# Optimization experiments

Hardware: AMD Instinct MI355X
Metric: run time of the kernel (lower is better)

## Reference

```python
import jax, jax.numpy as jnp
import numpy as np

B, S, D = 4, 1024, 1024
H = 16           # heads
HD = D // H      # head dim
E = 8            # experts
TOPK = 2
F = 4 * D        # expert ffn hidden


def setup_inputs() -> dict:
    key = jax.random.key(0)
    ks = jax.random.split(key, 8)
    w = lambda k, shp: jax.random.normal(k, shp, dtype=jnp.float32) * 0.02
    return {
        "x": jax.random.normal(ks[0], (B, S, D), dtype=jnp.float32),
        "ln1_g": jnp.ones((D,), jnp.float32), "ln1_b": jnp.zeros((D,), jnp.float32),
        "Wqkv": w(ks[1], (D, 3 * D)),
        "Wo": w(ks[2], (D, D)),
        "ln2_g": jnp.ones((D,), jnp.float32), "ln2_b": jnp.zeros((D,), jnp.float32),
        "Wg": w(ks[3], (D, E)),
        "W1": w(ks[4], (E, D, F)),
        "W2": w(ks[5], (E, F, D)),
    }


def _layernorm(x, g, b, eps=1e-5):
    mu = jnp.mean(x, axis=-1, keepdims=True)
    var = jnp.var(x, axis=-1, keepdims=True)
    return (x - mu) * jax.lax.rsqrt(var + eps) * g + b


def _attn(h, Wqkv, Wo):
    qkv = h @ Wqkv                                   # [B,S,3D]
    q, k, v = jnp.split(qkv, 3, axis=-1)
    q = q.reshape(B, S, H, HD)
    k = k.reshape(B, S, H, HD)
    v = v.reshape(B, S, H, HD)
    scores = jnp.einsum("bqhd,bkhd->bhqk", q, k) / np.sqrt(HD)
    causal = jnp.tril(jnp.ones((S, S), bool))
    scores = jnp.where(causal, scores, jnp.finfo(scores.dtype).min)
    p = jax.nn.softmax(scores, axis=-1)
    o = jnp.einsum("bhqk,bkhd->bqhd", p, v).reshape(B, S, D)
    return o @ Wo


def _moe(h, Wg, W1, W2):
    # h: [N, D] tokens; top-k softmax gating, dense all-expert reference
    logits = h @ Wg                                   # [N, E]
    top_vals, top_idx = jax.lax.top_k(logits, TOPK)   # [N, k]
    wts = jax.nn.softmax(top_vals, axis=-1)           # gate weights over top-k
    gates = jnp.sum(jax.nn.one_hot(top_idx, E) * wts[..., None], axis=1)  # [N, E]
    act = jax.nn.gelu(jnp.einsum("nd,edf->enf", h, W1))  # [E, N, F]
    eo = jnp.einsum("enf,efd->end", act, W2)             # [E, N, D]
    return jnp.einsum("ne,end->nd", gates, eo)           # combine


def reference(x, ln1_g, ln1_b, Wqkv, Wo, ln2_g, ln2_b, Wg, W1, W2):
    h = _layernorm(x, ln1_g, ln1_b)
    x_resid = x + _attn(h, Wqkv, Wo)
    moe_in = _layernorm(x_resid, ln2_g, ln2_b).reshape(B * S, D)
    y = _moe(moe_in, Wg, W1, W2).reshape(B, S, D)
    return x_resid + y
```

## Files before the change

kernel.cpp:

```cpp
#include <hip/hip_runtime.h>

typedef unsigned short u16;
typedef _Float16 f16x8 __attribute__((ext_vector_type(8)));
typedef __bf16   bf16x8 __attribute__((ext_vector_type(8)));
typedef float    f32x4 __attribute__((ext_vector_type(4)));

struct __align__(8) U16x4 { u16 v[4]; };

#define MAXT 72

__device__ __forceinline__ u16 f2b(float f) {
  unsigned u = __builtin_bit_cast(unsigned, f);
  return (u16)((u + 0x7FFFu + ((u >> 16) & 1u)) >> 16);
}
__device__ __forceinline__ u16 f2h(float f) { return __builtin_bit_cast(u16, (_Float16)f); }
__device__ __forceinline__ u16 f2h_lo(float f) {
  _Float16 h = (_Float16)f;
  return __builtin_bit_cast(u16, (_Float16)(f - (float)h));
}
__device__ __forceinline__ void llds16(const void* g, void* l) {
  __builtin_amdgcn_global_load_lds((const __attribute__((address_space(1))) unsigned int*)g,
                                   (__attribute__((address_space(3))) unsigned int*)l, 16, 0, 0);
}
__device__ __forceinline__ f32x4 mmf(f16x8 a, f16x8 b, f32x4 c) {
  return __builtin_amdgcn_mfma_f32_16x16x32_f16(a, b, c, 0, 0, 0);
}
__device__ __forceinline__ f32x4 mmb(bf16x8 a, bf16x8 b, f32x4 c) {
  return __builtin_amdgcn_mfma_f32_16x16x32_bf16(a, b, c, 0, 0, 0);
}

template<int OUT>
__global__ __launch_bounds__(256) void transpose_kernel(const float* __restrict__ src,
                                                        u16* __restrict__ d0, u16* __restrict__ d1,
                                                        int R, int C) {
  __shared__ float t[32][33];
  long zo = (long)blockIdx.z * R * C;
  int r0 = blockIdx.y << 5, c0 = blockIdx.x << 5;
  int tid = threadIdx.x;
  {
    int r = tid >> 3, c = (tid & 7) << 2;
    float4 v = *(const float4*)(src + zo + (long)(r0 + r) * C + c0 + c);
    t[r][c] = v.x; t[r][c + 1] = v.y; t[r][c + 2] = v.z; t[r][c + 3] = v.w;
  }
  __syncthreads();
  int c = tid >> 3, rg = (tid & 7) << 2;
  long o = zo + (long)(c0 + c) * R + r0 + rg;
  U16x4 a, b2;
#pragma unroll
  for (int i = 0; i < 4; i++) {
    float f = t[rg + i][c];
    if (OUT == 0) { a.v[i] = f2h(f); b2.v[i] = f2h_lo(f); }
    else a.v[i] = f2b(f);
  }
  *(U16x4*)(d0 + o) = a;
  if (OUT == 0) *(U16x4*)(d1 + o) = b2;
}

__global__ __launch_bounds__(256) void wg_transpose(const float* __restrict__ Wg,
                                                    float* __restrict__ WgT) {
  int idx = blockIdx.x * 256 + threadIdx.x;
  int d = idx >> 3, e = idx & 7;
  WgT[e * 1024 + d] = Wg[idx];
}

__global__ __launch_bounds__(256) void ln_kernel(const float* __restrict__ x, const float* __restrict__ g,
                                                 const float* __restrict__ bt,
                                                 u16* __restrict__ d0, u16* __restrict__ d1) {
  long row = blockIdx.x;
  int tid = threadIdx.x;
  const float4 v = *(const float4*)(x + (row << 10) + (tid << 2));
  float s = v.x + v.y + v.z + v.w;
  float q = v.x * v.x + v.y * v.y + v.z * v.z + v.w * v.w;
#pragma unroll
  for (int m = 1; m < 64; m <<= 1) { s += __shfl_xor(s, m); q += __shfl_xor(q, m); }
  __shared__ float rs[4], rq[4];
  if ((tid & 63) == 0) { rs[tid >> 6] = s; rq[tid >> 6] = q; }
  __syncthreads();
  s = rs[0] + rs[1] + rs[2] + rs[3];
  q = rq[0] + rq[1] + rq[2] + rq[3];
  float mu = s * (1.f / 1024.f);
  float inv = 1.f / sqrtf(q * (1.f / 1024.f) - mu * mu + 1e-5f);
  float4 gg = *(const float4*)(g + (tid << 2));
  float4 bb = *(const float4*)(bt + (tid << 2));
  float o0 = (v.x - mu) * inv * gg.x + bb.x;
  float o1 = (v.y - mu) * inv * gg.y + bb.y;
  float o2 = (v.z - mu) * inv * gg.z + bb.z;
  float o3 = (v.w - mu) * inv * gg.w + bb.w;
  long o = (row << 10) + (tid << 2);
  U16x4 a, b2;
  a.v[0] = f2h(o0); a.v[1] = f2h(o1); a.v[2] = f2h(o2); a.v[3] = f2h(o3);
  b2.v[0] = f2h_lo(o0); b2.v[1] = f2h_lo(o1); b2.v[2] = f2h_lo(o2); b2.v[3] = f2h_lo(o3);
  *(U16x4*)(d0 + o) = a; *(U16x4*)(d1 + o) = b2;
}

template<int MODE>
__global__ __launch_bounds__(512, 1) void gemm_kernel(
    const u16* __restrict__ Ah, const u16* __restrict__ Al,
    const u16* __restrict__ Bh, const u16* __restrict__ Bl,
    int K, int ldc, int Nexp,
    const int* __restrict__ lists, const int* __restrict__ tile_e,
    const int* __restrict__ tile_b, const int* __restrict__ tile_c,
    float* __restrict__ outf, u16* __restrict__ outb,
    const float* __restrict__ resid, const float* __restrict__ slotw) {
  constexpr bool SPLIT = (MODE < 2);
  constexpr int TN = (MODE == 1) ? 64 : 128;
  constexpr int NF = TN >> 6;
  constexpr int NB = TN >> 6;
  __shared__ u16 lds[4][8192];
  const int tid = threadIdx.x, w = tid >> 6, l = tid & 63;
  int n0;
  int grbase = 0, rowsv = 128;
  long m0 = 0;
  if (MODE >= 2) {
    int lin = blockIdx.x;
    int c = lin & 7, k = lin >> 3;
    int ty = c * 9 + (k % 9);
    int tx = k / 9;
    n0 = tx * TN;
    int e = tile_e[ty];
    if (e < 0) return;
    grbase = tile_b[ty];
    rowsv = tile_c[ty];
    Bh += (long)e * Nexp * K;
  } else {
    n0 = blockIdx.x * TN;
    m0 = (long)blockIdx.y << 7;
  }

  const u16 *as0[2], *as1[2], *bs0[2], *bs1[2];
  int dstA[2], dstB[2];
#pragma unroll
  for (int i = 0; i < 2; i++) {
    int chunk = i * 512 + tid;
    int row = chunk >> 3, c16 = chunk & 7;
    int scol = (c16 << 4) ^ ((row & 7) << 4);
    dstA[i] = chunk << 4;
    long ar;
    if (MODE == 2) {
      int vlu = lists[(row < rowsv) ? (grbase + row) : grbase];
      ar = (long)(vlu >> 1);
    } else if (MODE == 3) {
      ar = grbase + ((row < rowsv) ? row : 0);
    } else {
      ar = m0 + row;
    }
    long ao = ar * (long)K + (scol >> 1);
    as0[i] = Ah + ao;
    if (SPLIT) as1[i] = Al + ao;
  }
#pragma unroll
  for (int i = 0; i < NB; i++) {
    int chunk = i * 512 + tid;
    int row = chunk >> 3, c16 = chunk & 7;
    int scol = (c16 << 4) ^ ((row & 7) << 4);
    dstB[i] = chunk << 4;
    long bo = (long)(n0 + row) * K + (scol >> 1);
    bs0[i] = Bh + bo;
    if (SPLIT) bs1[i] = Bl + bo;
  }

  f32x4 acc[4][NF];
#pragma unroll
  for (int i = 0; i < 4; i++)
#pragma unroll
    for (int j = 0; j < NF; j++) acc[i][j] = (f32x4){0.f, 0.f, 0.f, 0.f};

  const int wr = (w >> 2) << 6;
  const int wc = (w & 3) * (TN / 4);
  const int nkt = K >> 6;

  if constexpr (SPLIT) {
    for (int kt = 0; kt < nkt; ++kt) {
      if (kt) __syncthreads();
#pragma unroll
      for (int i = 0; i < 2; i++) {
        llds16(as0[i] + (kt << 6), (char*)(&lds[0][0]) + dstA[i]);
        llds16(as1[i] + (kt << 6), (char*)(&lds[2][0]) + dstA[i]);
      }
#pragma unroll
      for (int i = 0; i < NB; i++) {
        llds16(bs0[i] + (kt << 6), (char*)(&lds[1][0]) + dstB[i]);
        llds16(bs1[i] + (kt << 6), (char*)(&lds[3][0]) + dstB[i]);
      }
      __syncthreads();
#pragma unroll
      for (int kc = 0; kc < 2; kc++) {
        const int kby = (kc << 6) + ((l >> 4) << 4);
        int aoff[4], boff[NF];
#pragma unroll
        for (int mf = 0; mf < 4; mf++) { int row = wr + (mf << 4) + (l & 15); aoff[mf] = (row << 7) + (kby ^ ((row & 7) << 4)); }
#pragma unroll
        for (int nf = 0; nf < NF; nf++) { int row = wc + (nf << 4) + (l & 15); boff[nf] = (row << 7) + (kby ^ ((row & 7) << 4)); }
        f16x8 a0[4], a1[4], b0[NF], b1[NF];
#pragma unroll
        for (int mf = 0; mf < 4; mf++) {
          a0[mf] = *(const f16x8*)((const char*)(&lds[0][0]) + aoff[mf]);
          a1[mf] = *(const f16x8*)((const char*)(&lds[2][0]) + aoff[mf]);
        }
#pragma unroll
        for (int nf = 0; nf < NF; nf++) {
          b0[nf] = *(const f16x8*)((const char*)(&lds[1][0]) + boff[nf]);
          b1[nf] = *(const f16x8*)((const char*)(&lds[3][0]) + boff[nf]);
        }
#pragma unroll
        for (int mf = 0; mf < 4; mf++)
#pragma unroll
          for (int nf = 0; nf < NF; nf++) {
            acc[mf][nf] = mmf(a0[mf], b0[nf], acc[mf][nf]);
            acc[mf][nf] = mmf(a0[mf], b1[nf], acc[mf][nf]);
            acc[mf][nf] = mmf(a1[mf], b0[nf], acc[mf][nf]);
          }
      }
    }
  } else {
#pragma unroll
    for (int i = 0; i < 2; i++) llds16(as0[i], (char*)(&lds[0][0]) + dstA[i]);
#pragma unroll
    for (int i = 0; i < NB; i++) llds16(bs0[i], (char*)(&lds[1][0]) + dstB[i]);
    __syncthreads();
    int cur = 0;
    for (int kt = 0; kt < nkt; ++kt) {
      if (kt + 1 < nkt) {
        const int nb = (cur ^ 1) << 1;
#pragma unroll
        for (int i = 0; i < 2; i++) llds16(as0[i] + ((kt + 1) << 6), (char*)(&lds[nb][0]) + dstA[i]);
#pragma unroll
        for (int i = 0; i < NB; i++) llds16(bs0[i] + ((kt + 1) << 6), (char*)(&lds[nb + 1][0]) + dstB[i]);
      }
      const char* pA = (const char*)(&lds[cur << 1][0]);
      const char* pB = (const char*)(&lds[(cur << 1) + 1][0]);
#pragma unroll
      for (int kc = 0; kc < 2; kc++) {
        const int kby = (kc << 6) + ((l >> 4) << 4);
        bf16x8 a0[4], b0[NF];
#pragma unroll
        for (int mf = 0; mf < 4; mf++) {
          int row = wr + (mf << 4) + (l & 15);
          a0[mf] = *(const bf16x8*)(pA + (row << 7) + (kby ^ ((row & 7) << 4)));
        }
#pragma unroll
        for (int nf = 0; nf < NF; nf++) {
          int row = wc + (nf << 4) + (l & 15);
          b0[nf] = *(const bf16x8*)(pB + (row << 7) + (kby ^ ((row & 7) << 4)));
        }
#pragma unroll
        for (int mf = 0; mf < 4; mf++)
#pragma unroll
          for (int nf = 0; nf < NF; nf++) acc[mf][nf] = mmb(a0[mf], b0[nf], acc[mf][nf]);
      }
      __syncthreads();
      cur ^= 1;
    }
  }

#pragma unroll
  for (int mf = 0; mf < 4; mf++) {
#pragma unroll
    for (int r = 0; r < 4; r++) {
      const int lrow = wr + (mf << 4) + ((l >> 4) << 2) + r;
      if (MODE >= 2 && lrow >= rowsv) continue;
      float gw = 0.f; long orow = 0;
      if (MODE == 3) { int gr = grbase + lrow; orow = (long)lists[gr] * ldc; gw = slotw[gr]; }
#pragma unroll
      for (int nf = 0; nf < NF; nf++) {
        const int col = n0 + wc + (nf << 4) + (l & 15);
        float v = acc[mf][nf][r];
        if (MODE == 0) {
          outf[(m0 + lrow) * (long)ldc + col] = v;
        } else if (MODE == 1) {
          long ix = (m0 + lrow) * (long)ldc + col;
          outf[ix] = v + resid[ix];
        } else if (MODE == 2) {
          float t = v * (1.59576912f + 0.07135539f * v * v);
          float u = v * __builtin_amdgcn_rcpf(1.f + __expf(-t));
          outb[(long)(grbase + lrow) * ldc + col] = f2b(u);
        } else {
          outf[orow + col] = v * gw;
        }
      }
    }
  }
}

__global__ __launch_bounds__(256) void kv_prep(const float* __restrict__ qkv,
                                               u16* __restrict__ Kh, u16* __restrict__ Kl,
                                               u16* __restrict__ Vth, u16* __restrict__ Vtl) {
  __shared__ float t[64][65];
  const int tid = threadIdx.x;
  const int kb = blockIdx.x, h = blockIdx.y, b = blockIdx.z;
  const long bb = ((long)b) << 10;
  const int hoff = h << 6;
  const long head = ((long)(b * 16 + h)) << 16;
  {
    int rr = tid >> 4, c = (tid & 15) << 2;
#pragma unroll
    for (int p = 0; p < 4; p++) {
      int r = rr + p * 16;
      const float* base = qkv + (bb + kb * 64 + r) * 3072 + hoff + c;
      float4 u = *(const float4*)(base + 1024);
      U16x4 a, lo;
      a.v[0] = f2h(u.x); a.v[1] = f2h(u.y); a.v[2] = f2h(u.z); a.v[3] = f2h(u.w);
      lo.v[0] = f2h_lo(u.x); lo.v[1] = f2h_lo(u.y); lo.v[2] = f2h_lo(u.z); lo.v[3] = f2h_lo(u.w);
      long o = head + (long)(kb * 64 + r) * 64 + c;
      *(U16x4*)(Kh + o) = a; *(U16x4*)(Kl + o) = lo;
      float4 v = *(const float4*)(base + 2048);
      t[r][c] = v.x; t[r][c + 1] = v.y; t[r][c + 2] = v.z; t[r][c + 3] = v.w;
    }
  }
  __syncthreads();
  {
    int hd = tid >> 2, k4 = (tid & 3) << 4;
#pragma unroll
    for (int q = 0; q < 4; q++) {
      U16x4 a, lo;
#pragma unroll
      for (int j = 0; j < 4; j++) {
        float f = t[k4 + q * 4 + j][hd];
        a.v[j] = f2h(f); lo.v[j] = f2h_lo(f);
      }
      long o = head + (long)hd * 1024 + kb * 64 + k4 + q * 4;
      *(U16x4*)(Vth + o) = a; *(U16x4*)(Vtl + o) = lo;
    }
  }
}

__global__ __launch_bounds__(256, 1) void attn_kernel(const float* __restrict__ qkv,
                                                      const u16* __restrict__ Kh, const u16* __restrict__ Kl,
                                                      const u16* __restrict__ Vth, const u16* __restrict__ Vtl,
                                                      u16* __restrict__ oh, u16* __restrict__ ol) {
  __shared__ u16 kh[4096], kl[4096];
  __shared__ u16 vh[4096], vl[4096];
  __shared__ u16 ph[4][1024], pl[4][1024];
  const int tid = threadIdx.x, w = tid >> 6, l = tid & 63;
  const int qbi = blockIdx.x, hh_ = blockIdx.y, b = blockIdx.z;
  const long bb = ((long)b) << 10;
  const int hoff = hh_ << 6;
  const long head = ((long)(b * 16 + hh_)) << 16;

  const u16 *ks0[2], *ks1[2], *vs0[2], *vs1[2];
  int db[2];
#pragma unroll
  for (int i = 0; i < 2; i++) {
    int chunk = i * 256 + tid;
    int row = chunk >> 3, c16 = chunk & 7;
    int sc = ((c16 << 4) ^ ((row & 7) << 4)) >> 1;
    db[i] = chunk << 4;
    ks0[i] = Kh + head + row * 64 + sc;
    ks1[i] = Kl + head + row * 64 + sc;
    vs0[i] = Vth + head + (long)row * 1024 + sc;
    vs1[i] = Vtl + head + (long)row * 1024 + sc;
  }

  for (int pass = 0; pass < 2; ++pass) {
    const int qb = (pass ? qbi : (15 - qbi)) << 6;
    f16x8 q0[2], q1[2];
    {
      const long qrow = bb + qb + (w << 4) + (l & 15);
      const float* qp = qkv + qrow * 3072 + hoff + ((l >> 4) << 3);
#pragma unroll
      for (int kc = 0; kc < 2; kc++) {
        float4 u0 = *(const float4*)(qp + (kc << 5));
        float4 u1 = *(const float4*)(qp + (kc << 5) + 4);
        float vv[8] = {u0.x, u0.y, u0.z, u0.w, u1.x, u1.y, u1.z, u1.w};
#pragma unroll
        for (int j = 0; j < 8; j++) {
          _Float16 hi = (_Float16)vv[j];
          q0[kc][j] = hi;
          q1[kc][j] = (_Float16)(vv[j] - (float)hi);
        }
      }
    }

    f32x4 o[4];
#pragma unroll
    for (int nf = 0; nf < 4; nf++) o[nf] = (f32x4){0.f, 0.f, 0.f, 0.f};
    float mr[4] = {-1e30f, -1e30f, -1e30f, -1e30f};
    float lr[4] = {0.f, 0.f, 0.f, 0.f};
    const int ktm = qb >> 6;

    for (int kt = 0; kt <= ktm; ++kt) {
      __syncthreads();
#pragma unroll
      for (int i = 0; i < 2; i++) {
        llds16(ks0[i] + (kt << 12), (char*)kh + db[i]);
        llds16(ks1[i] + (kt << 12), (char*)kl + db[i]);
        llds16(vs0[i] + (kt << 6), (char*)vh + db[i]);
        llds16(vs1[i] + (kt << 6), (char*)vl + db[i]);
      }
      __syncthreads();

      f32x4 s[4];
#pragma unroll
      for (int nf = 0; nf < 4; nf++) s[nf] = (f32x4){0.f, 0.f, 0.f, 0.f};
#pragma unroll
      for (int kc = 0; kc < 2; kc++) {
        const int kby = (kc << 6) + ((l >> 4) << 4);
#pragma unroll
        for (int nf = 0; nf < 4; nf++) {
          int row = (nf << 4) + (l & 15);
          int off = (row << 7) + (kby ^ ((row & 7) << 4));
          f16x8 k0 = *(const f16x8*)((const char*)kh + off);
          f16x8 k1 = *(const f16x8*)((const char*)kl + off);
          s[nf] = mmf(q0[kc], k0, s[nf]);
          s[nf] = mmf(q0[kc], k1, s[nf]);
          s[nf] = mmf(q1[kc], k0, s[nf]);
        }
      }
      const bool lastt = (kt == ktm);
#pragma unroll
      for (int nf = 0; nf < 4; nf++)
#pragma unroll
        for (int r = 0; r < 4; r++) {
          float sc = s[nf][r] * 0.125f;
          if (lastt) {
            int keyg = (kt << 6) + (nf << 4) + (l & 15);
            int qg = qb + (w << 4) + ((l >> 4) << 2) + r;
            if (keyg > qg) sc = -1e30f;
          }
          s[nf][r] = sc;
        }
      float alpha[4];
#pragma unroll
      for (int r = 0; r < 4; r++) {
        float mx = fmaxf(fmaxf(s[0][r], s[1][r]), fmaxf(s[2][r], s[3][r]));
        mx = fmaxf(mx, __shfl_xor(mx, 1));
        mx = fmaxf(mx, __shfl_xor(mx, 2));
        mx = fmaxf(mx, __shfl_xor(mx, 4));
        mx = fmaxf(mx, __shfl_xor(mx, 8));
        float mn = fmaxf(mr[r], mx);
        float su = 0.f;
#pragma unroll
        for (int nf = 0; nf < 4; nf++) { float pv = __expf(s[nf][r] - mn); s[nf][r] = pv; su += pv; }
        su += __shfl_xor(su, 1); su += __shfl_xor(su, 2);
        su += __shfl_xor(su, 4); su += __shfl_xor(su, 8);
        alpha[r] = __expf(mr[r] - mn);
        lr[r] = lr[r] * alpha[r] + su;
        mr[r] = mn;
      }
#pragma unroll
      for (int nf = 0; nf < 4; nf++)
#pragma unroll
        for (int r = 0; r < 4; r++) o[nf][r] *= alpha[r];
#pragma unroll
      for (int nf = 0; nf < 4; nf++)
#pragma unroll
        for (int r = 0; r < 4; r++) {
          int m = ((l >> 4) << 2) + r, k = (nf << 4) + (l & 15);
          int off = (m << 7) + ((k << 1) ^ ((m & 7) << 4));
          float pv = s[nf][r];
          _Float16 hi = (_Float16)pv;
          *(u16*)((char*)&ph[w][0] + off) = __builtin_bit_cast(u16, hi);
          *(u16*)((char*)&pl[w][0] + off) = __builtin_bit_cast(u16, (_Float16)(pv - (float)hi));
        }
#pragma unroll
      for (int kc = 0; kc < 2; kc++) {
        const int kby = (kc << 6) + ((l >> 4) << 4);
        const int mm = l & 15;
        int poff = (mm << 7) + (kby ^ ((mm & 7) << 4));
        f16x8 p0 = *(const f16x8*)((const char*)&ph[w][0] + poff);
        f16x8 p1 = *(const f16x8*)((const char*)&pl[w][0] + poff);
#pragma unroll
        for (int nf = 0; nf < 4; nf++) {
          int row = (nf << 4) + (l & 15);
          int off = (row << 7) + (kby ^ ((row & 7) << 4));
          f16x8 v0 = *(const f16x8*)((const char*)vh + off);
          f16x8 v1 = *(const f16x8*)((const char*)vl + off);
          o[nf] = mmf(p0, v0, o[nf]);
          o[nf] = mmf(p0, v1, o[nf]);
          o[nf] = mmf(p1, v0, o[nf]);
        }
      }
    }
#pragma unroll
    for (int nf = 0; nf < 4; nf++)
#pragma unroll
      for (int r = 0; r < 4; r++) {
        int lrow = (w << 4) + ((l >> 4) << 2) + r;
        float v = o[nf][r] / lr[r];
        long ix = (bb + qb + lrow) * 1024 + hoff + (nf << 4) + (l & 15);
        _Float16 hi = (_Float16)v;
        oh[ix] = __builtin_bit_cast(u16, hi);
        ol[ix] = __builtin_bit_cast(u16, (_Float16)(v - (float)hi));
      }
  }
}

__global__ __launch_bounds__(256) void gate_kernel(const float* __restrict__ xr, const float* __restrict__ g,
                                                   const float* __restrict__ b, const float* __restrict__ WgT,
                                                   int* __restrict__ tok_e, float* __restrict__ tok_w,
                                                   u16* __restrict__ moe) {
  int w = threadIdx.x >> 6, l = threadIdx.x & 63;
  long t = (long)blockIdx.x * 4 + w;
  const float* row = xr + (t << 10);
  float4 xv[4]; float s = 0.f, q = 0.f;
#pragma unroll
  for (int i = 0; i < 4; i++) {
    float4 v = *(const float4*)(row + (i << 8) + (l << 2));
    xv[i] = v;
    s += v.x + v.y + v.z + v.w;
    q += v.x * v.x + v.y * v.y + v.z * v.z + v.w * v.w;
  }
#pragma unroll
  for (int m = 1; m < 64; m <<= 1) { s += __shfl_xor(s, m); q += __shfl_xor(q, m); }
  float mu = s * (1.f / 1024.f);
  float inv = 1.f / sqrtf(q * (1.f / 1024.f) - mu * mu + 1e-5f);
  float acc[8] = {0.f, 0.f, 0.f, 0.f, 0.f, 0.f, 0.f, 0.f};
#pragma unroll
  for (int i = 0; i < 4; i++) {
    int d0 = (i << 8) + (l << 2);
    float4 gg = *(const float4*)(g + d0);
    float4 bb = *(const float4*)(b + d0);
    float x0 = (xv[i].x - mu) * inv * gg.x + bb.x;
    float x1 = (xv[i].y - mu) * inv * gg.y + bb.y;
    float x2 = (xv[i].z - mu) * inv * gg.z + bb.z;
    float x3 = (xv[i].w - mu) * inv * gg.w + bb.w;
    U16x4 st;
    st.v[0] = f2b(x0); st.v[1] = f2b(x1); st.v[2] = f2b(x2); st.v[3] = f2b(x3);
    *(U16x4*)(moe + (t << 10) + d0) = st;
#pragma unroll
    for (int e = 0; e < 8; e++) {
      float4 wq = *(const float4*)(WgT + (e << 10) + d0);
      acc[e] += x0 * wq.x + x1 * wq.y + x2 * wq.z + x3 * wq.w;
    }
  }
#pragma unroll
  for (int e = 0; e < 8; e++)
#pragma unroll
    for (int m = 1; m < 64; m <<= 1) acc[e] += __shfl_xor(acc[e], m);
  if (l == 0) {
    int e0 = 0; float v0 = acc[0];
#pragma unroll
    for (int e = 1; e < 8; e++) if (acc[e] > v0) { v0 = acc[e]; e0 = e; }
    int e1 = (e0 == 0) ? 1 : 0; float v1 = acc[e1];
#pragma unroll
    for (int e = 0; e < 8; e++) if (e != e0 && acc[e] > v1) { v1 = acc[e]; e1 = e; }
    float w0 = 1.f / (1.f + __expf(v1 - v0));
    tok_e[t * 2] = e0; tok_e[t * 2 + 1] = e1;
    tok_w[t * 2] = w0; tok_w[t * 2 + 1] = 1.f - w0;
  }
}

__global__ __launch_bounds__(256) void plan_kernel(const int* __restrict__ tok_e, int* __restrict__ cursor,
                                                   int* __restrict__ tile_e, int* __restrict__ tile_b,
                                                   int* __restrict__ tile_c) {
  __shared__ int wc[4][8];
  int tid = threadIdx.x, w = tid >> 6, l = tid & 63;
  int c0 = 0, c1 = 0, c2 = 0, c3 = 0, c4 = 0, c5 = 0, c6 = 0, c7 = 0;
  for (int k = 0; k < 32; k++) {
    int v = tok_e[(w << 11) + (k << 6) + l];
    c0 += (v == 0); c1 += (v == 1); c2 += (v == 2); c3 += (v == 3);
    c4 += (v == 4); c5 += (v == 5); c6 += (v == 6); c7 += (v == 7);
  }
#pragma unroll
  for (int m = 1; m < 64; m <<= 1) {
    c0 += __shfl_xor(c0, m); c1 += __shfl_xor(c1, m); c2 += __shfl_xor(c2, m); c3 += __shfl_xor(c3, m);
    c4 += __shfl_xor(c4, m); c5 += __shfl_xor(c5, m); c6 += __shfl_xor(c6, m); c7 += __shfl_xor(c7, m);
  }
  if (l == 0) {
    wc[w][0] = c0; wc[w][1] = c1; wc[w][2] = c2; wc[w][3] = c3;
    wc[w][4] = c4; wc[w][5] = c5; wc[w][6] = c6; wc[w][7] = c7;
  }
  __syncthreads();
  if (tid == 0) {
    int o = 0, t2 = 0;
    for (int e = 0; e < 8; e++) {
      cursor[e] = o;
      int cc = wc[0][e] + wc[1][e] + wc[2][e] + wc[3][e];
      for (int i = 0; i < cc; i += 128) {
        tile_e[t2] = e; tile_b[t2] = o + i; tile_c[t2] = (cc - i < 128) ? (cc - i) : 128; t2++;
      }
      o += cc;
    }
    for (; t2 < MAXT; t2++) tile_e[t2] = -1;
  }
}

__global__ __launch_bounds__(256) void scatter_kernel(const int* __restrict__ tok_e, const float* __restrict__ tok_w,
                                                      int* __restrict__ cursor, int* __restrict__ lists,
                                                      float* __restrict__ slotw) {
  int t = blockIdx.x * 256 + threadIdx.x;
#pragma unroll
  for (int s = 0; s < 2; s++) {
    int e = tok_e[t * 2 + s];
    int pos = atomicAdd(&cursor[e], 1);
    lists[pos] = t * 2 + s;
    slotw[pos] = tok_w[t * 2 + s];
  }
}

__global__ __launch_bounds__(256) void combine_kernel(float* __restrict__ out, const float* __restrict__ yp) {
  long i = (long)blockIdx.x * 256 + threadIdx.x;
  long n = i >> 8;
  long d = i & 255;
  float4 o = *(float4*)(out + (i << 2));
  const float4 a = *(const float4*)(yp + ((n * 2) << 10) + (d << 2));
  const float4 b = *(const float4*)(yp + ((n * 2 + 1) << 10) + (d << 2));
  o.x += a.x + b.x; o.y += a.y + b.y; o.z += a.z + b.z; o.w += a.w + b.w;
  *(float4*)(out + (i << 2)) = o;
}

extern "C" void kernel_launch(void* const* d_in, const int* in_sizes, int n_in,
                              void* d_out, int out_size, void* d_ws, size_t ws_size,
                              hipStream_t stream) {
  const float* x    = (const float*)d_in[0];
  const float* ln1g = (const float*)d_in[1];
  const float* ln1b = (const float*)d_in[2];
  const float* Wqkv = (const float*)d_in[3];
  const float* Wo   = (const float*)d_in[4];
  const float* ln2g = (const float*)d_in[5];
  const float* ln2b = (const float*)d_in[6];
  const float* Wg   = (const float*)d_in[7];
  const float* W1   = (const float*)d_in[8];
  const float* W2   = (const float*)d_in[9];
  float* out = (float*)d_out;
  char* ws = (char*)d_ws;

  size_t off = 0;
  auto alloc = [&](size_t b) { size_t o = off; off += (b + 255) & ~size_t(255); return o; };
  u16* WqkvTh = (u16*)(ws + alloc(3072ull * 1024 * 2));
  u16* WqkvTl = (u16*)(ws + alloc(3072ull * 1024 * 2));
  u16* WoTh   = (u16*)(ws + alloc(1024ull * 1024 * 2));
  u16* WoTl   = (u16*)(ws + alloc(1024ull * 1024 * 2));
  u16* W1T    = (u16*)(ws + alloc(8ull * 4096 * 1024 * 2));
  u16* W2T    = (u16*)(ws + alloc(8ull * 1024 * 4096 * 2));
  u16* hh     = (u16*)(ws + alloc(4096ull * 1024 * 2));
  u16* hl     = (u16*)(ws + alloc(4096ull * 1024 * 2));
  float* qkv  = (float*)(ws + alloc(4096ull * 3072 * 4));
  u16* atth   = (u16*)(ws + alloc(4096ull * 1024 * 2));
  u16* attl   = (u16*)(ws + alloc(4096ull * 1024 * 2));
  u16* moein  = (u16*)(ws + alloc(4096ull * 1024 * 2));
  u16* act    = (u16*)(ws + alloc(8192ull * 4096 * 2));
  float* WgT  = (float*)(ws + alloc(8ull * 1024 * 4));
  float* ypart = qkv;
  u16* Kh  = act;
  u16* Kl  = act + 4194304;
  u16* Vth = act + 2 * 4194304;
  u16* Vtl = act + 3 * 4194304;
  int* tok_e  = (int*)(ws + alloc(8192 * 4));
  float* tok_w = (float*)(ws + alloc(8192 * 4));
  int* cursor = (int*)(ws + alloc(64));
  int* lists  = (int*)(ws + alloc(8192 * 4));
  float* slotw = (float*)(ws + alloc(8192 * 4));
  int* tile_e = (int*)(ws + alloc(MAXT * 4));
  int* tile_b = (int*)(ws + alloc(MAXT * 4));
  int* tile_c = (int*)(ws + alloc(MAXT * 4));
  (void)in_sizes; (void)n_in; (void)out_size; (void)ws_size;

  dim3 blk(256), blk512(512);
  transpose_kernel<0><<<dim3(96, 32, 1), blk, 0, stream>>>(Wqkv, WqkvTh, WqkvTl, 1024, 3072);
  transpose_kernel<0><<<dim3(32, 32, 1), blk, 0, stream>>>(Wo, WoTh, WoTl, 1024, 1024);
  transpose_kernel<1><<<dim3(128, 32, 8), blk, 0, stream>>>(W1, W1T, nullptr, 1024, 4096);
  transpose_kernel<1><<<dim3(32, 128, 8), blk, 0, stream>>>(W2, W2T, nullptr, 4096, 1024);
  wg_transpose<<<dim3(32), blk, 0, stream>>>(Wg, WgT);
  ln_kernel<<<dim3(4096), blk, 0, stream>>>(x, ln1g, ln1b, hh, hl);
  gemm_kernel<0><<<dim3(24, 32), blk512, 0, stream>>>(hh, hl, WqkvTh, WqkvTl, 1024, 3072, 0,
                                                      nullptr, nullptr, nullptr, nullptr,
                                                      qkv, nullptr, nullptr, nullptr);
  kv_prep<<<dim3(16, 16, 4), blk, 0, stream>>>(qkv, Kh, Kl, Vth, Vtl);
  attn_kernel<<<dim3(8, 16, 4), blk, 0, stream>>>(qkv, Kh, Kl, Vth, Vtl, atth, attl);
  gemm_kernel<1><<<dim3(16, 32), blk512, 0, stream>>>(atth, attl, WoTh, WoTl, 1024, 1024, 0,
                                                      nullptr, nullptr, nullptr, nullptr,
                                                      out, nullptr, x, nullptr);
  gate_kernel<<<dim3(1024), blk, 0, stream>>>(out, ln2g, ln2b, WgT, tok_e, tok_w, moein);
  plan_kernel<<<dim3(1), blk, 0, stream>>>(tok_e, cursor, tile_e, tile_b, tile_c);
  scatter_kernel<<<dim3(16), blk, 0, stream>>>(tok_e, tok_w, cursor, lists, slotw);
  gemm_kernel<2><<<dim3(8 * 9 * 32), blk512, 0, stream>>>(moein, nullptr, W1T, nullptr, 1024, 4096, 4096,
                                                          lists, tile_e, tile_b, tile_c,
                                                          nullptr, act, nullptr, nullptr);
  gemm_kernel<3><<<dim3(8 * 9 * 8), blk512, 0, stream>>>(act, nullptr, W2T, nullptr, 4096, 1024, 1024,
                                                         lists, tile_e, tile_b, tile_c,
                                                         ypart, nullptr, nullptr, slotw);
  combine_kernel<<<dim3(4096), blk, 0, stream>>>(out, ypart);
}
```

Measured before the change: 568.3 us.

## Prefetch two k-tiles ahead in MoE down-proj GEMM; single-buffer the up-proj GEMM

For MODE 3 (the expert W2 GEMM with scatter-combine), the kernel now keeps a double-buffered LDS pipeline that issues loads two k-steps ahead. It uses explicit vmcnt waits and raw s_barrier instead of __syncthreads, so global-to-LDS transfers overlap with MFMA work. MODE 2 falls back to a single-buffered load-then-compute loop and its LDS shrinks to 32 KB. The LDS is now a byte array sized per mode. This could let more blocks fit per CU for MODE 2, but that mode loses its prefetch overlap, and the hand-written waitcnt counting depends on exact instruction counts.

Result: faster. 547.4 us (-3.7%).

```diff
diff --git a/kernel.cpp b/kernel.cpp
--- a/kernel.cpp
+++ b/kernel.cpp
@@ -106,7 +106,8 @@
   constexpr int TN = (MODE == 1) ? 64 : 128;
   constexpr int NF = TN >> 6;
   constexpr int NB = TN >> 6;
-  __shared__ u16 lds[4][8192];
+  constexpr int SMEM = (MODE == 2) ? 32768 : 65536;
+  __shared__ __align__(16) char smem[SMEM];
   const int tid = threadIdx.x, w = tid >> 6, l = tid & 63;
   int n0;
   int grbase = 0, rowsv = 128;
@@ -169,18 +170,67 @@
   const int wc = (w & 3) * (TN / 4);
   const int nkt = K >> 6;
 
-  if constexpr (SPLIT) {
+  if constexpr (MODE == 3) {
+#pragma unroll
+    for (int i = 0; i < 2; i++) llds16(as0[i], smem + dstA[i]);
+#pragma unroll
+    for (int i = 0; i < 2; i++) llds16(bs0[i], smem + 16384 + dstB[i]);
+    asm volatile("" ::: "memory");
+#pragma unroll
+    for (int i = 0; i < 2; i++) llds16(as0[i] + 64, smem + 32768 + dstA[i]);
+#pragma unroll
+    for (int i = 0; i < 2; i++) llds16(bs0[i] + 64, smem + 49152 + dstB[i]);
+    for (int kt = 0; kt < nkt; ++kt) {
+      const int cur = kt & 1;
+      if (kt + 1 < nkt) asm volatile("s_waitcnt vmcnt(4)" ::: "memory");
+      else              asm volatile("s_waitcnt vmcnt(0)" ::: "memory");
+      asm volatile("s_barrier" ::: "memory");
+      const char* pA = (const char*)smem + (cur << 15);
+      const char* pB = pA + 16384;
+#pragma unroll
+      for (int kc = 0; kc < 2; kc++) {
+        const int kby = (kc << 6) + ((l >> 4) << 4);
+        bf16x8 a0[4], b0[NF];
+#pragma unroll
+        for (int mf = 0; mf < 4; mf++) {
+          int row = wr + (mf << 4) + (l & 15);
+          a0[mf] = *(const bf16x8*)(pA + (row << 7) + (kby ^ ((row & 7) << 4)));
+        }
+#pragma unroll
+        for (int nf = 0; nf < NF; nf++) {
+          int row = wc + (nf << 4) + (l & 15);
+          b0[nf] = *(const bf16x8*)(pB + (row << 7) + (kby ^ ((row & 7) << 4)));
+        }
+#pragma unroll
+        for (int mf = 0; mf < 4; mf++)
+#pragma unroll
+          for (int nf = 0; nf < NF; nf++) acc[mf][nf] = mmb(a0[mf], b0[nf], acc[mf][nf]);
+      }
+      asm volatile("s_barrier" ::: "memory");
+      if (kt + 2 < nkt) {
+        char* qa = (char*)smem + (cur << 15);
+#pragma unroll
+        for (int i = 0; i < 2; i++) llds16(as0[i] + ((kt + 2) << 6), qa + dstA[i]);
+#pragma unroll
+        for (int i = 0; i < 2; i++) llds16(bs0[i] + ((kt + 2) << 6), qa + 16384 + dstB[i]);
+      }
+    }
+  } else {
+    char* pAh = smem;
+    char* pBh = smem + 16384;
+    char* pAl = smem + 32768;
+    char* pBl = smem + 49152;
     for (int kt = 0; kt < nkt; ++kt) {
       if (kt) __syncthreads();
 #pragma unroll
       for (int i = 0; i < 2; i++) {
-        llds16(as0[i] + (kt << 6), (char*)(&lds[0][0]) + dstA[i]);
-        llds16(as1[i] + (kt << 6), (char*)(&lds[2][0]) + dstA[i]);
+        llds16(as0[i] + (kt << 6), pAh + dstA[i]);
+        if (SPLIT) llds16(as1[i] + (kt << 6), pAl + dstA[i]);
       }
 #pragma unroll
       for (int i = 0; i < NB; i++) {
-        llds16(bs0[i] + (kt << 6), (char*)(&lds[1][0]) + dstB[i]);
-        llds16(bs1[i] + (kt << 6), (char*)(&lds[3][0]) + dstB[i]);
+        llds16(bs0[i] + (kt << 6), pBh + dstB[i]);
+        if (SPLIT) llds16(bs1[i] + (kt << 6), pBl + dstB[i]);
       }
       __syncthreads();
 #pragma unroll
@@ -191,65 +241,38 @@
         for (int mf = 0; mf < 4; mf++) { int row = wr + (mf << 4) + (l & 15); aoff[mf] = (row << 7) + (kby ^ ((row & 7) << 4)); }
 #pragma unroll
         for (int nf = 0; nf < NF; nf++) { int row = wc + (nf << 4) + (l & 15); boff[nf] = (row << 7) + (kby ^ ((row & 7) << 4)); }
-        f16x8 a0[4], a1[4], b0[NF], b1[NF];
-#pragma unroll
-        for (int mf = 0; mf < 4; mf++) {
-          a0[mf] = *(const f16x8*)((const char*)(&lds[0][0]) + aoff[mf]);
-          a1[mf] = *(const f16x8*)((const char*)(&lds[2][0]) + aoff[mf]);
-        }
-#pragma unroll
-        for (int nf = 0; nf < NF; nf++) {
-          b0[nf] = *(const f16x8*)((const char*)(&lds[1][0]) + boff[nf]);
-          b1[nf] = *(const f16x8*)((const char*)(&lds[3][0]) + boff[nf]);
-        }
-#pragma unroll
-        for (int mf = 0; mf < 4; mf++)
+        if (SPLIT) {
+          f16x8 a0[4], a1[4], b0[NF], b1[NF];
+#pragma unroll
+          for (int mf = 0; mf < 4; mf++) {
+            a0[mf] = *(const f16x8*)(pAh + aoff[mf]);
+            a1[mf] = *(const f16x8*)(pAl + aoff[mf]);
+          }
 #pragma unroll
           for (int nf = 0; nf < NF; nf++) {
-            acc[mf][nf] = mmf(a0[mf], b0[nf], acc[mf][nf]);
-            acc[mf][nf] = mmf(a0[mf], b1[nf], acc[mf][nf]);
-            acc[mf][nf] = mmf(a1[mf], b0[nf], acc[mf][nf]);
+            b0[nf] = *(const f16x8*)(pBh + boff[nf]);
+            b1[nf] = *(const f16x8*)(pBl + boff[nf]);
           }
-      }
-    }
-  } else {
-#pragma unroll
-    for (int i = 0; i < 2; i++) llds16(as0[i], (char*)(&lds[0][0]) + dstA[i]);
-#pragma unroll
-    for (int i = 0; i < NB; i++) llds16(bs0[i], (char*)(&lds[1][0]) + dstB[i]);
-    __syncthreads();
-    int cur = 0;
-    for (int kt = 0; kt < nkt; ++kt) {
-      if (kt + 1 < nkt) {
-        const int nb = (cur ^ 1) << 1;
-#pragma unroll
-        for (int i = 0; i < 2; i++) llds16(as0[i] + ((kt + 1) << 6), (char*)(&lds[nb][0]) + dstA[i]);
-#pragma unroll
-        for (int i = 0; i < NB; i++) llds16(bs0[i] + ((kt + 1) << 6), (char*)(&lds[nb + 1][0]) + dstB[i]);
-      }
-      const char* pA = (const char*)(&lds[cur << 1][0]);
-      const char* pB = (const char*)(&lds[(cur << 1) + 1][0]);
-#pragma unroll
-      for (int kc = 0; kc < 2; kc++) {
-        const int kby = (kc << 6) + ((l >> 4) << 4);
-        bf16x8 a0[4], b0[NF];
-#pragma unroll
-        for (int mf = 0; mf < 4; mf++) {
-          int row = wr + (mf << 4) + (l & 15);
-          a0[mf] = *(const bf16x8*)(pA + (row << 7) + (kby ^ ((row & 7) << 4)));
-        }
-#pragma unroll
-        for (int nf = 0; nf < NF; nf++) {
-          int row = wc + (nf << 4) + (l & 15);
-          b0[nf] = *(const bf16x8*)(pB + (row << 7) + (kby ^ ((row & 7) << 4)));
-        }
-#pragma unroll
-        for (int mf = 0; mf < 4; mf++)
-#pragma unroll
-          for (int nf = 0; nf < NF; nf++) acc[mf][nf] = mmb(a0[mf], b0[nf], acc[mf][nf]);
-      }
-      __syncthreads();
-      cur ^= 1;
+#pragma unroll
+          for (int mf = 0; mf < 4; mf++)
+#pragma unroll
+            for (int nf = 0; nf < NF; nf++) {
+              acc[mf][nf] = mmf(a0[mf], b0[nf], acc[mf][nf]);
+              acc[mf][nf] = mmf(a0[mf], b1[nf], acc[mf][nf]);
+              acc[mf][nf] = mmf(a1[mf], b0[nf], acc[mf][nf]);
+            }
+        } else {
+          bf16x8 a0[4], b0[NF];
+#pragma unroll
+          for (int mf = 0; mf < 4; mf++) a0[mf] = *(const bf16x8*)(pAh + aoff[mf]);
+#pragma unroll
+          for (int nf = 0; nf < NF; nf++) b0[nf] = *(const bf16x8*)(pBh + boff[nf]);
+#pragma unroll
+          for (int mf = 0; mf < 4; mf++)
+#pragma unroll
+            for (int nf = 0; nf < NF; nf++) acc[mf][nf] = mmb(a0[mf], b0[nf], acc[mf][nf]);
+        }
+      }
     }
   }
 
```
